# Performance work log

Measured on AMD Instinct MI355X. Metric: run time of the kernel, lower is better.

Reference implementation:

```python
import jax, jax.numpy as jnp
import numpy as np
from jax import lax

TAU = 2.0
V_TH = 1.0
SG_ALPHA = 4.0  # spikingjelly default sigmoid surrogate alpha


def lif_multistep(x):
    """Multi-step LIF with hard reset to 0, v_init=0, detach_reset=True.
    x: (T, ...). Returns binary spikes (same shape), with sigmoid surrogate
    gradient injected via straight-through estimator.
    """
    def step(v, xt):
        h = v + (xt - v) / TAU                      # membrane charge
        s_hard = (h >= V_TH).astype(h.dtype)        # heaviside spike
        sur = jax.nn.sigmoid(SG_ALPHA * (h - V_TH))  # surrogate for grad
        s = s_hard + (sur - lax.stop_gradient(sur))  # fwd=hard, bwd=surrogate
        v_next = h * (1.0 - lax.stop_gradient(s))    # hard reset, detached
        return v_next, s
    _, spikes = lax.scan(step, jnp.zeros_like(x[0]), x)
    return spikes


def setup_inputs() -> dict:
    key = jax.random.key(0)
    ks = jax.random.split(key, 6)
    T, B, N, D = 4, 16, 197, 512
    w_std = 1.0 / np.sqrt(D)
    return {
        "x":  jax.random.normal(ks[0], (T, B, N, D), dtype=jnp.float32),
        "Wq": jax.random.normal(ks[1], (D, D), dtype=jnp.float32) * w_std,
        "Wk": jax.random.normal(ks[2], (D, D), dtype=jnp.float32) * w_std,
        "Wv": jax.random.normal(ks[3], (D, D), dtype=jnp.float32) * w_std,
        "Wp": jax.random.normal(ks[4], (D, D), dtype=jnp.float32) * w_std,
        "bp": jnp.zeros((D,), dtype=jnp.float32),
    }


def reference(x, Wq, Wk, Wv, Wp, bp):
    T, B, N, D = x.shape
    H = 8
    dh = D // H
    scale = dh ** -0.5

    # QKV projections (nn.Linear: x @ W.T, no bias)
    q = jnp.einsum('tbnd,ed->tbne', x, Wq)
    k = jnp.einsum('tbnd,ed->tbne', x, Wk)
    v = jnp.einsum('tbnd,ed->tbne', x, Wv)

    # LIF spiking over timestep dim T -> binary spike tensors
    qs = lif_multistep(q).reshape(T, B, N, H, dh).transpose(0, 1, 3, 2, 4)
    ks_ = lif_multistep(k).reshape(T, B, N, H, dh).transpose(0, 1, 3, 2, 4)
    vs = lif_multistep(v).reshape(T, B, N, H, dh).transpose(0, 1, 3, 2, 4)

    # spike-driven attention: binary matmul, no softmax
    attn = jnp.einsum('tbhnd,tbhmd->tbhnm', qs, ks_) * scale  # (T,B,H,N,N)
    attn_map = lax.stop_gradient(attn)
    out = jnp.einsum('tbhnm,tbhmd->tbhnd', attn, vs)          # (T,B,H,N,dh)
    out = out.transpose(0, 1, 3, 2, 4).reshape(T, B, N, D)

    # output projection + LIF
    out = jnp.einsum('tbnd,ed->tbne', out, Wp) + bp
    out = lif_multistep(out)
    return out, attn_map
```

## Files before the change

### kernel.cpp

```cpp
#include <hip/hip_runtime.h>
#include <stdint.h>

#define T_ 4
#define B_ 16
#define N_ 197
#define D_ 512
#define H_ 8
#define DH 64
#define BN_ (B_*N_)
#define PLANE (BN_*D_)
#define M_ (T_*BN_)
#define TENSOR_ELEMS (T_*PLANE)
#define WELEMS (D_*D_)
#define MH (M_*H_)
#define FLAG_TOL 6e-3f
#define NFW3 (3*PLANE/64)
#define NFWP (PLANE/64)

typedef __attribute__((ext_vector_type(8))) short short8v;
typedef __attribute__((ext_vector_type(8))) _Float16 f16x8;
typedef __attribute__((ext_vector_type(4))) float f32x4;
typedef __attribute__((ext_vector_type(16))) float f32x16;
typedef __attribute__((ext_vector_type(4))) unsigned short ushort4v;
typedef unsigned long long u64;
typedef unsigned int u32;

__device__ __forceinline__ ushort f16_bits(float f) {
    _Float16 h = (_Float16)f;
    return __builtin_bit_cast(unsigned short, h);
}
__device__ __forceinline__ float f16_val(ushort u) {
    return (float)__builtin_bit_cast(_Float16, u);
}

__device__ __forceinline__ void gload16(const void* g, void* l) {
    __builtin_amdgcn_global_load_lds(
        (const __attribute__((address_space(1))) unsigned int*)g,
        (__attribute__((address_space(3))) unsigned int*)l, 16, 0, 0);
}

__global__ void cvt16(const float* __restrict__ src, ushort* __restrict__ dst, int n)
{
    int i = (blockIdx.x*256 + threadIdx.x)*4;
    if (i >= n) return;
    float4 v = *(const float4*)(src + i);
    ushort4v o;
    o[0] = f16_bits(v.x); o[1] = f16_bits(v.y);
    o[2] = f16_bits(v.z); o[3] = f16_bits(v.w);
    *(ushort4v*)(dst + i) = o;
}

__global__ __launch_bounds__(256, 4)
void gemm_qkv_lif(const ushort* __restrict__ xh, const ushort* __restrict__ w3h,
                  u64* __restrict__ bits3, u64* __restrict__ fmap3)
{
    __shared__ __align__(16) ushort smem[16384];
    const int tid = threadIdx.x;
    const int lane = tid & 63, wn = tid >> 6;
    const int l31 = lane & 31, lg = lane >> 5;
    const int nyz = 12, nz = 3;

    int nwg = gridDim.x, orig = blockIdx.x;
    int q8 = nwg >> 3, r8 = nwg & 7, xcd = orig & 7, loc = orig >> 3;
    int wg = (xcd < r8 ? xcd*(q8+1) : r8*(q8+1) + (xcd-r8)*q8) + loc;
    int bx = wg / nyz, yz = wg - bx*nyz;
    int by = yz / nz,  z  = yz - by*nz;

    const int bm0 = bx * 32;
    const int bn0 = by * 128;
    const ushort* Wz = w3h + (size_t)z * WELEMS;

    f32x16 acc[4];
    #pragma unroll
    for (int t = 0; t < 4; ++t)
        #pragma unroll
        for (int r = 0; r < 16; ++r) acc[t][r] = 0.f;

    for (int kt = 0; kt < D_; kt += 64) {
        #pragma unroll
        for (int i = 0; i < 8; ++i) {
            const int q = ((i & 3) << 8) | tid;
            const int row = q & 127, c = q >> 7;
            ushort* dst = smem + ((i >> 2) << 13) + q*8;
            if (i < 4) {
                int t = row >> 5, r32 = row & 31;
                if (bm0 + r32 < BN_)
                    gload16(xh + ((size_t)(t*BN_ + bm0 + r32)*D_ + kt + c*8), dst);
            } else {
                gload16(Wz + ((size_t)(bn0 + row)*D_ + kt + c*8), dst);
            }
        }
        __syncthreads();
        #pragma unroll
        for (int s = 0; s < 4; ++s) {
            const int cA = (s << 1) | lg;
            f16x8 bv = *(const f16x8*)&smem[8192 + (cA*128 + wn*32 + l31)*8];
            #pragma unroll
            for (int t = 0; t < 4; ++t) {
                f16x8 av = *(const f16x8*)&smem[(cA*128 + t*32 + l31)*8];
                acc[t] = __builtin_amdgcn_mfma_f32_32x32x16_f16(av, bv, acc[t], 0, 0, 0);
            }
        }
        __syncthreads();
    }

    u32* sp = (u32*)smem;
    u32* fl = (u32*)smem + 512;
    #pragma unroll
    for (int r = 0; r < 16; ++r) {
        bool s[4]; bool fg = false; float v = 0.f;
        #pragma unroll
        for (int t = 0; t < 4; ++t) {
            float h = v + (acc[t][r] - v)*0.5f;
            s[t] = h >= 1.0f;
            fg |= fabsf(h - 1.0f) < FLAG_TOL;
            v = s[t] ? 0.f : h;
        }
        #pragma unroll
        for (int t = 0; t < 4; ++t) {
            u64 m = __ballot(s[t]);
            if (lane == 0) {
                sp[((wn*4 + t)*16 + r)*2 + 0] = (u32)m;
                sp[((wn*4 + t)*16 + r)*2 + 1] = (u32)(m >> 32);
            }
        }
        u64 fm = __ballot(fg);
        if (lane == 0) {
            fl[(wn*16 + r)*2 + 0] = (u32)fm;
            fl[(wn*16 + r)*2 + 1] = (u32)(fm >> 32);
        }
    }
    __syncthreads();
    {
        int t = tid >> 6, row32 = (tid >> 1) & 31, hl = tid & 1;
        int rr = (row32 & 3) | ((row32 >> 3) << 2);
        int lgg = (row32 >> 2) & 1;
        u64 word = (u64)sp[(((2*hl)*4 + t)*16 + rr)*2 + lgg]
                 | ((u64)sp[(((2*hl+1)*4 + t)*16 + rr)*2 + lgg] << 32);
        if (bm0 + row32 < BN_)
            bits3[(size_t)z*MH + (size_t)(t*BN_ + bm0 + row32)*H_ + (bn0 >> 6) + hl] = word;
        if (tid < 64) {
            int rowf = tid >> 1, hlf = tid & 1;
            int rf = (rowf & 3) | ((rowf >> 3) << 2);
            int lgf = (rowf >> 2) & 1;
            u64 fw = (u64)fl[((2*hlf)*16 + rf)*2 + lgf]
                   | ((u64)fl[((2*hlf+1)*16 + rf)*2 + lgf] << 32);
            if (bm0 + rowf < BN_)
                fmap3[(size_t)z*NFWP + (size_t)(bm0 + rowf)*8 + (bn0 >> 6) + hlf] = fw;
        }
    }
}

__global__ __launch_bounds__(256, 4)
void gemm_proj_lif(const ushort* __restrict__ oh, const ushort* __restrict__ wph,
                   const float* __restrict__ bias, float* __restrict__ outp,
                   u64* __restrict__ fmapp)
{
    __shared__ __align__(16) ushort smem[16384];
    const int tid = threadIdx.x;
    const int lane = tid & 63, wn = tid >> 6;
    const int l31 = lane & 31, lg = lane >> 5;
    const int nyz = 4;

    int nwg = gridDim.x, orig = blockIdx.x;
    int q8 = nwg >> 3, r8 = nwg & 7, xcd = orig & 7, loc = orig >> 3;
    int wg = (xcd < r8 ? xcd*(q8+1) : r8*(q8+1) + (xcd-r8)*q8) + loc;
    int bx = wg / nyz, by = wg - bx*nyz;

    const int bm0 = bx * 32, bn0 = by * 128;

    f32x16 acc[4];
    #pragma unroll
    for (int t = 0; t < 4; ++t)
        #pragma unroll
        for (int r = 0; r < 16; ++r) acc[t][r] = 0.f;

    for (int kt = 0; kt < D_; kt += 64) {
        #pragma unroll
        for (int i = 0; i < 8; ++i) {
            const int q = ((i & 3) << 8) | tid;
            const int row = q & 127, c = q >> 7;
            ushort* dst = smem + ((i >> 2) << 13) + q*8;
            if (i < 4) {
                int t = row >> 5, r32 = row & 31;
                if (bm0 + r32 < BN_)
                    gload16(oh + ((size_t)(t*BN_ + bm0 + r32)*D_ + kt + c*8), dst);
            } else {
                gload16(wph + ((size_t)(bn0 + row)*D_ + kt + c*8), dst);
            }
        }
        __syncthreads();
        #pragma unroll
        for (int s = 0; s < 4; ++s) {
            const int cA = (s << 1) | lg;
            f16x8 bv = *(const f16x8*)&smem[8192 + (cA*128 + wn*32 + l31)*8];
            #pragma unroll
            for (int t = 0; t < 4; ++t) {
                f16x8 av = *(const f16x8*)&smem[(cA*128 + t*32 + l31)*8];
                acc[t] = __builtin_amdgcn_mfma_f32_32x32x16_f16(av, bv, acc[t], 0, 0, 0);
            }
        }
        __syncthreads();
    }

    const int gcol = bn0 + wn*32 + l31;
    const float bb = bias[gcol];
    u32* fl = (u32*)smem;
    #pragma unroll
    for (int r = 0; r < 16; ++r) {
        const int row32 = (r & 3) + 8*(r >> 2) + 4*lg;
        const bool live = bm0 + row32 < BN_;
        bool fg = false; float v = 0.f;
        #pragma unroll
        for (int t = 0; t < 4; ++t) {
            float h = v + ((acc[t][r] + bb) - v)*0.5f;
            bool st = h >= 1.0f;
            fg |= fabsf(h - 1.0f) < FLAG_TOL;
            if (live)
                outp[(size_t)t*PLANE + (size_t)(bm0 + row32)*D_ + gcol] = st ? 1.0f : 0.0f;
            v = st ? 0.f : h;
        }
        u64 fm = __ballot(fg);
        if (lane == 0) {
            fl[(wn*16 + r)*2 + 0] = (u32)fm;
            fl[(wn*16 + r)*2 + 1] = (u32)(fm >> 32);
        }
    }
    __syncthreads();
    if (tid < 64) {
        int rowf = tid >> 1, hlf = tid & 1;
        int rf = (rowf & 3) | ((rowf >> 3) << 2);
        int lgf = (rowf >> 2) & 1;
        u64 fw = (u64)fl[((2*hlf)*16 + rf)*2 + lgf]
               | ((u64)fl[((2*hlf+1)*16 + rf)*2 + lgf] << 32);
        if (bm0 + rowf < BN_)
            fmapp[(size_t)(bm0 + rowf)*8 + (bn0 >> 6) + hlf] = fw;
    }
}

__global__ __launch_bounds__(256)
void fixup_qkv(const float* __restrict__ x,
               const float* __restrict__ Wq, const float* __restrict__ Wk,
               const float* __restrict__ Wv,
               u64* __restrict__ bits3, const u64* __restrict__ flagmap)
{
    const int lane = threadIdx.x & 63;
    const int wv = blockIdx.x*4 + (threadIdx.x >> 6);
    const int nw = gridDim.x*4;
    for (int w = wv; w < NFW3; w += nw) {
        u64 fm = flagmap[w];
        while (fm) {
            int bit = __ffsll((long long)fm) - 1;
            fm &= fm - 1;
            int id = (w << 6) + bit;
            int tsr = id / PLANE;
            int rem = id - tsr*PLANE;
            int r = rem >> 9, e = rem & (D_-1);
            const float* W = (tsr==0) ? Wq : (tsr==1 ? Wk : Wv);
            const float* wr = W + (size_t)e*D_;
            u64* bits = bits3 + (size_t)tsr*MH;
            float wv8[8];
            #pragma unroll
            for (int i = 0; i < 8; ++i) wv8[i] = wr[lane + 64*i];
            double dots[T_];
            #pragma unroll
            for (int t = 0; t < T_; ++t) {
                const float* xr = x + (size_t)(t*BN_ + r)*D_;
                float xv8[8];
                #pragma unroll
                for (int i = 0; i < 8; ++i) xv8[i] = xr[lane + 64*i];
                double p = 0.0;
                #pragma unroll
                for (int i = 0; i < 8; ++i) p += (double)xv8[i]*(double)wv8[i];
                dots[t] = p;
            }
            #pragma unroll
            for (int off = 32; off > 0; off >>= 1)
                #pragma unroll
                for (int t = 0; t < T_; ++t)
                    dots[t] += __shfl_down(dots[t], off);
            if (lane == 0) {
                double v = 0.0;
                u64 b = 1ull << (e & 63);
                #pragma unroll
                for (int t = 0; t < T_; ++t) {
                    double hh = v + (dots[t] - v)/2.0;
                    bool s = hh >= 1.0;
                    size_t wd = (size_t)(t*BN_ + r)*H_ + (e >> 6);
                    if (s) atomicOr(&bits[wd], b);
                    else   atomicAnd(&bits[wd], ~b);
                    v = s ? 0.0 : hh;
                }
            }
        }
    }
}

#define NP 208
#define QSTR 72
#define JP 224
#define VSTR 232

__global__ __launch_bounds__(256)
void attn_qk(const u64* __restrict__ qbits, const u64* __restrict__ kbits,
             float* __restrict__ attn_out)
{
    __shared__ ushort Qs[NP][QSTR];
    __shared__ ushort Ks[NP][QSTR];
    int tb = blockIdx.x, h = blockIdx.y;
    int tid = threadIdx.x, wave = tid >> 6, lane = tid & 63;

    for (int idx = tid; idx < NP*16; idx += 256) {
        int j = idx >> 4, d4 = (idx & 15) << 2;
        ushort qv[4] = {0,0,0,0}, kv[4] = {0,0,0,0};
        if (j < N_) {
            size_t w = ((size_t)tb*N_ + j)*H_ + h;
            u64 qw = qbits[w], kw = kbits[w];
            #pragma unroll
            for (int r = 0; r < 4; ++r) {
                qv[r] = ((qw >> (d4+r)) & 1ull) ? 0x3F80 : 0;
                kv[r] = ((kw >> (d4+r)) & 1ull) ? 0x3F80 : 0;
            }
        }
        #pragma unroll
        for (int r = 0; r < 4; ++r) { Qs[j][d4+r] = qv[r]; Ks[j][d4+r] = kv[r]; }
    }
    __syncthreads();

    const int il = lane & 15;
    const int kk = (lane >> 4) << 3;
    const int ig = (lane >> 4) << 2;
    const size_t amap = ((size_t)tb*H_ + h)*(size_t)(N_*N_);

    for (int it = wave; it < 13; it += 4) {
        int i0 = it << 4;
        short8v a0 = *(const short8v*)&Qs[i0 + il][kk];
        short8v a1 = *(const short8v*)&Qs[i0 + il][kk + 32];
        for (int jt = 0; jt < 13; ++jt) {
            int j0 = jt << 4;
            short8v b0 = *(const short8v*)&Ks[j0 + il][kk];
            short8v b1 = *(const short8v*)&Ks[j0 + il][kk + 32];
            f32x4 c = {0.f, 0.f, 0.f, 0.f};
            c = __builtin_amdgcn_mfma_f32_16x16x32_bf16(a0, b0, c, 0, 0, 0);
            c = __builtin_amdgcn_mfma_f32_16x16x32_bf16(a1, b1, c, 0, 0, 0);
            int j = j0 + il;
            if (j < N_) {
                #pragma unroll
                for (int r = 0; r < 4; ++r) {
                    int i = i0 + ig + r;
                    if (i < N_) attn_out[amap + (size_t)i*N_ + j] = c[r]*0.125f;
                }
            }
        }
    }
}

__global__ __launch_bounds__(256)
void attn_pv(const float* __restrict__ attn, const u64* __restrict__ vbits,
             ushort* __restrict__ of16)
{
    __shared__ ushort Vt[DH][VSTR];
    int tb = blockIdx.x, h = blockIdx.y, zh = blockIdx.z;
    int tid = threadIdx.x, wave = tid >> 6, lane = tid & 63;

    for (int idx = tid; idx < JP*16; idx += 256) {
        int j = idx >> 4, d4 = (idx & 15) << 2;
        ushort vv[4] = {0,0,0,0};
        if (j < N_) {
            u64 vw = vbits[((size_t)tb*N_ + j)*H_ + h];
            #pragma unroll
            for (int r = 0; r < 4; ++r)
                vv[r] = ((vw >> (d4+r)) & 1ull) ? 0x3F80 : 0;
        }
        Vt[d4+0][j]=vv[0]; Vt[d4+1][j]=vv[1]; Vt[d4+2][j]=vv[2]; Vt[d4+3][j]=vv[3];
    }
    __syncthreads();

    const int il = lane & 15, kk = (lane >> 4) << 3, ig = (lane >> 4) << 2;
    const size_t amap = ((size_t)tb*H_ + h)*(size_t)(N_*N_);

    const int it_lo = zh*7 + wave;
    const int it_hi = zh*7 + 7 < 13 ? zh*7 + 7 : 13;
    for (int it = it_lo; it < it_hi; it += 4) {
        int i0 = it << 4;
        int row = i0 + il; if (row > N_-1) row = N_-1;
        const float* arow = attn + amap + (size_t)row*N_;
        f32x4 o[4];
        #pragma unroll
        for (int dt = 0; dt < 4; ++dt) o[dt] = (f32x4){0.f,0.f,0.f,0.f};
        #pragma unroll
        for (int kt = 0; kt < 7; ++kt) {
            const int c0 = kt*32 + kk;
            float f[8];
            if (kt < 6) {
                float4 fa = *(const float4*)(arow + c0);
                float4 fb = *(const float4*)(arow + c0 + 4);
                f[0]=fa.x; f[1]=fa.y; f[2]=fa.z; f[3]=fa.w;
                f[4]=fb.x; f[5]=fb.y; f[6]=fb.z; f[7]=fb.w;
            } else {
                #pragma unroll
                for (int j = 0; j < 8; ++j)
                    f[j] = (c0 + j < N_) ? arow[c0 + j] : 0.f;
            }
            short8v a;
            #pragma unroll
            for (int j = 0; j < 8; ++j)
                a[j] = (short)(__float_as_uint(f[j]) >> 16);
            #pragma unroll
            for (int dt = 0; dt < 4; ++dt) {
                short8v b = *(const short8v*)&Vt[dt*16 + il][c0];
                o[dt] = __builtin_amdgcn_mfma_f32_16x16x32_bf16(a, b, o[dt], 0, 0, 0);
            }
        }
        #pragma unroll
        for (int dt = 0; dt < 4; ++dt)
            #pragma unroll
            for (int r = 0; r < 4; ++r) {
                int i = i0 + ig + r;
                if (i < N_)
                    of16[((size_t)tb*N_ + i)*D_ + (size_t)h*DH + dt*16 + il] =
                        f16_bits(o[dt][r]);
            }
    }
}

__global__ __launch_bounds__(256)
void fixup_proj(const ushort* __restrict__ of16, const float* __restrict__ Wp,
                const float* __restrict__ bp, float* __restrict__ outp,
                const u64* __restrict__ flagmap)
{
    const int lane = threadIdx.x & 63;
    const int wv = blockIdx.x*4 + (threadIdx.x >> 6);
    const int nw = gridDim.x*4;
    for (int w = wv; w < NFWP; w += nw) {
        u64 fm = flagmap[w];
        while (fm) {
            int bit = __ffsll((long long)fm) - 1;
            fm &= fm - 1;
            int rem = (w << 6) + bit;
            int r = rem >> 9, e = rem & (D_-1);
            const float* wr = Wp + (size_t)e*D_;
            float wv8[8];
            #pragma unroll
            for (int i = 0; i < 8; ++i) wv8[i] = wr[lane + 64*i];
            double dots[T_];
            #pragma unroll
            for (int t = 0; t < T_; ++t) {
                const ushort* ar = of16 + (size_t)(t*BN_ + r)*D_;
                float av8[8];
                #pragma unroll
                for (int i = 0; i < 8; ++i) av8[i] = f16_val(ar[lane + 64*i]);
                double p = 0.0;
                #pragma unroll
                for (int i = 0; i < 8; ++i) p += (double)av8[i]*(double)wv8[i];
                dots[t] = p;
            }
            #pragma unroll
            for (int off = 32; off > 0; off >>= 1)
                #pragma unroll
                for (int t = 0; t < T_; ++t)
                    dots[t] += __shfl_down(dots[t], off);
            if (lane == 0) {
                double v = 0.0;
                #pragma unroll
                for (int t = 0; t < T_; ++t) {
                    double xt = dots[t] + (double)bp[e];
                    double h = v + (xt - v)/2.0;
                    bool s = h >= 1.0;
                    outp[(size_t)t*PLANE + rem] = s ? 1.0f : 0.0f;
                    v = s ? 0.0 : h;
                }
            }
        }
    }
}

extern "C" void kernel_launch(void* const* d_in, const int* in_sizes, int n_in,
                              void* d_out, int out_size, void* d_ws, size_t ws_size,
                              hipStream_t stream)
{
    const float* x  = (const float*)d_in[0];
    const float* Wq = (const float*)d_in[1];
    const float* Wk = (const float*)d_in[2];
    const float* Wv = (const float*)d_in[3];
    const float* Wp = (const float*)d_in[4];
    const float* bp = (const float*)d_in[5];
    float* out_spk  = (float*)d_out;
    float* attn_out = (float*)d_out + TENSOR_ELEMS;

    char* ws = (char*)d_ws;
    const size_t BUFB = (size_t)TENSOR_ELEMS * sizeof(float);
    if (ws_size < 4*BUFB) return;
    ushort* of16 = (ushort*)(ws + 2*BUFB);
    char* r3 = ws + 3*BUFB;
    ushort* xh   = (ushort*)r3;
    ushort* w3h  = (ushort*)(r3 + (13u<<20));
    ushort* wph  = (ushort*)(r3 + (15u<<20));
    u64*    bits3 = (u64*)(r3 + (16u<<20));
    u64*    qbits = bits3;
    u64*    kbits = bits3 + MH;
    u64*    vbits = bits3 + 2*(size_t)MH;
    u64*    fmap3 = (u64*)(r3 + (19u<<20));
    u64*    fmapp = (u64*)(r3 + (20u<<20));

    cvt16<<<TENSOR_ELEMS/1024, 256, 0, stream>>>(x, xh, TENSOR_ELEMS);
    cvt16<<<WELEMS/1024, 256, 0, stream>>>(Wq, w3h,            WELEMS);
    cvt16<<<WELEMS/1024, 256, 0, stream>>>(Wk, w3h +   WELEMS, WELEMS);
    cvt16<<<WELEMS/1024, 256, 0, stream>>>(Wv, w3h + 2*WELEMS, WELEMS);
    cvt16<<<WELEMS/1024, 256, 0, stream>>>(Wp, wph,            WELEMS);

    gemm_qkv_lif<<<99*12, 256, 0, stream>>>(xh, w3h, bits3, fmap3);
    fixup_qkv<<<2048, 256, 0, stream>>>(x, Wq, Wk, Wv, bits3, fmap3);

    attn_qk<<<dim3(T_*B_, H_), 256, 0, stream>>>(qbits, kbits, attn_out);
    attn_pv<<<dim3(T_*B_, H_, 2), 256, 0, stream>>>(attn_out, vbits, of16);

    gemm_proj_lif<<<99*4, 256, 0, stream>>>(of16, wph, bp, out_spk, fmapp);
    fixup_proj<<<1024, 256, 0, stream>>>(of16, Wp, bp, out_spk, fmapp);
}
```

Measured before the change: 181.5 us.

## Double-buffer GEMM LDS staging and fuse QK and PV attention kernels

Both projection GEMMs now use two LDS buffers, issuing the next K-tile's global-to-LDS loads before computing on the current one. This is meant to overlap memory latency with MFMA work, at the cost of doubling shared memory and dropping the occupancy hint from launch bounds. Separately, the QK and PV attention kernels are merged into one. Each wave computes its row tile of scores, writes them to the attention map, and keeps a bf16 copy in LDS for the PV MFMA, so the fp32 attention map is no longer re-read from global memory. The fused kernel launches half as many blocks as the old PV kernel, which risks lower parallelism.

```diff
diff --git a/kernel.cpp b/kernel.cpp
--- a/kernel.cpp
+++ b/kernel.cpp
@@ -39,6 +39,14 @@
         (__attribute__((address_space(3))) unsigned int*)l, 16, 0, 0);
 }
 
+__device__ __forceinline__ short8v unpack8(u32 bits) {
+    short8v r;
+    #pragma unroll
+    for (int j = 0; j < 8; ++j)
+        r[j] = (short)(((bits >> j) & 1u) ? 0x3F80 : 0);
+    return r;
+}
+
 __global__ void cvt16(const float* __restrict__ src, ushort* __restrict__ dst, int n)
 {
     int i = (blockIdx.x*256 + threadIdx.x)*4;
@@ -50,11 +58,11 @@
     *(ushort4v*)(dst + i) = o;
 }
 
-__global__ __launch_bounds__(256, 4)
+__global__ __launch_bounds__(256)
 void gemm_qkv_lif(const ushort* __restrict__ xh, const ushort* __restrict__ w3h,
                   u64* __restrict__ bits3, u64* __restrict__ fmap3)
 {
-    __shared__ __align__(16) ushort smem[16384];
+    __shared__ __align__(16) ushort smem[32768];
     const int tid = threadIdx.x;
     const int lane = tid & 63, wn = tid >> 6;
     const int l31 = lane & 31, lg = lane >> 5;
@@ -76,12 +84,12 @@
         #pragma unroll
         for (int r = 0; r < 16; ++r) acc[t][r] = 0.f;
 
-    for (int kt = 0; kt < D_; kt += 64) {
+    auto STAGE = [&](int buf, int kt) {
         #pragma unroll
         for (int i = 0; i < 8; ++i) {
             const int q = ((i & 3) << 8) | tid;
             const int row = q & 127, c = q >> 7;
-            ushort* dst = smem + ((i >> 2) << 13) + q*8;
+            ushort* dst = smem + buf*16384 + ((i >> 2) << 13) + q*8;
             if (i < 4) {
                 int t = row >> 5, r32 = row & 31;
                 if (bm0 + r32 < BN_)
@@ -90,18 +98,30 @@
                 gload16(Wz + ((size_t)(bn0 + row)*D_ + kt + c*8), dst);
             }
         }
-        __syncthreads();
+    };
+    auto COMPUTE = [&](int buf) {
+        const ushort* base = smem + buf*16384;
         #pragma unroll
         for (int s = 0; s < 4; ++s) {
             const int cA = (s << 1) | lg;
-            f16x8 bv = *(const f16x8*)&smem[8192 + (cA*128 + wn*32 + l31)*8];
+            f16x8 bv = *(const f16x8*)&base[8192 + (cA*128 + wn*32 + l31)*8];
             #pragma unroll
             for (int t = 0; t < 4; ++t) {
-                f16x8 av = *(const f16x8*)&smem[(cA*128 + t*32 + l31)*8];
+                f16x8 av = *(const f16x8*)&base[(cA*128 + t*32 + l31)*8];
                 acc[t] = __builtin_amdgcn_mfma_f32_32x32x16_f16(av, bv, acc[t], 0, 0, 0);
             }
         }
+    };
+
+    STAGE(0, 0);
+    __syncthreads();
+    int cur = 0;
+    #pragma unroll
+    for (int k64 = 0; k64 < 8; ++k64) {
+        if (k64 < 7) STAGE(cur ^ 1, (k64 + 1)*64);
+        COMPUTE(cur);
         __syncthreads();
+        cur ^= 1;
     }
 
     u32* sp = (u32*)smem;
@@ -151,12 +171,12 @@
     }
 }
 
-__global__ __launch_bounds__(256, 4)
+__global__ __launch_bounds__(256)
 void gemm_proj_lif(const ushort* __restrict__ oh, const ushort* __restrict__ wph,
                    const float* __restrict__ bias, float* __restrict__ outp,
                    u64* __restrict__ fmapp)
 {
-    __shared__ __align__(16) ushort smem[16384];
+    __shared__ __align__(16) ushort smem[32768];
     const int tid = threadIdx.x;
     const int lane = tid & 63, wn = tid >> 6;
     const int l31 = lane & 31, lg = lane >> 5;
@@ -175,12 +195,12 @@
         #pragma unroll
         for (int r = 0; r < 16; ++r) acc[t][r] = 0.f;
 
-    for (int kt = 0; kt < D_; kt += 64) {
+    auto STAGE = [&](int buf, int kt) {
         #pragma unroll
         for (int i = 0; i < 8; ++i) {
             const int q = ((i & 3) << 8) | tid;
             const int row = q & 127, c = q >> 7;
-            ushort* dst = smem + ((i >> 2) << 13) + q*8;
+            ushort* dst = smem + buf*16384 + ((i >> 2) << 13) + q*8;
             if (i < 4) {
                 int t = row >> 5, r32 = row & 31;
                 if (bm0 + r32 < BN_)
@@ -189,18 +209,30 @@
                 gload16(wph + ((size_t)(bn0 + row)*D_ + kt + c*8), dst);
             }
         }
-        __syncthreads();
+    };
+    auto COMPUTE = [&](int buf) {
+        const ushort* base = smem + buf*16384;
         #pragma unroll
         for (int s = 0; s < 4; ++s) {
             const int cA = (s << 1) | lg;
-            f16x8 bv = *(const f16x8*)&smem[8192 + (cA*128 + wn*32 + l31)*8];
+            f16x8 bv = *(const f16x8*)&base[8192 + (cA*128 + wn*32 + l31)*8];
             #pragma unroll
             for (int t = 0; t < 4; ++t) {
-                f16x8 av = *(const f16x8*)&smem[(cA*128 + t*32 + l31)*8];
+                f16x8 av = *(const f16x8*)&base[(cA*128 + t*32 + l31)*8];
                 acc[t] = __builtin_amdgcn_mfma_f32_32x32x16_f16(av, bv, acc[t], 0, 0, 0);
             }
         }
+    };
+
+    STAGE(0, 0);
+    __syncthreads();
+    int cur = 0;
+    #pragma unroll
+    for (int k64 = 0; k64 < 8; ++k64) {
+        if (k64 < 7) STAGE(cur ^ 1, (k64 + 1)*64);
+        COMPUTE(cur);
         __syncthreads();
+        cur ^= 1;
     }
 
     const int gcol = bn0 + wn*32 + l31;
@@ -296,71 +328,17 @@
     }
 }
 
-#define NP 208
-#define QSTR 72
 #define JP 224
 #define VSTR 232
 
 __global__ __launch_bounds__(256)
-void attn_qk(const u64* __restrict__ qbits, const u64* __restrict__ kbits,
-             float* __restrict__ attn_out)
-{
-    __shared__ ushort Qs[NP][QSTR];
-    __shared__ ushort Ks[NP][QSTR];
+void attn_fused(const u64* __restrict__ qbits, const u64* __restrict__ kbits,
+                const u64* __restrict__ vbits,
+                float* __restrict__ attn_out, ushort* __restrict__ of16)
+{
+    __shared__ ushort Vt[DH][VSTR];
+    __shared__ ushort Ss[4][16][VSTR];
     int tb = blockIdx.x, h = blockIdx.y;
-    int tid = threadIdx.x, wave = tid >> 6, lane = tid & 63;
-
-    for (int idx = tid; idx < NP*16; idx += 256) {
-        int j = idx >> 4, d4 = (idx & 15) << 2;
-        ushort qv[4] = {0,0,0,0}, kv[4] = {0,0,0,0};
-        if (j < N_) {
-            size_t w = ((size_t)tb*N_ + j)*H_ + h;
-            u64 qw = qbits[w], kw = kbits[w];
-            #pragma unroll
-            for (int r = 0; r < 4; ++r) {
-                qv[r] = ((qw >> (d4+r)) & 1ull) ? 0x3F80 : 0;
-                kv[r] = ((kw >> (d4+r)) & 1ull) ? 0x3F80 : 0;
-            }
-        }
-        #pragma unroll
-        for (int r = 0; r < 4; ++r) { Qs[j][d4+r] = qv[r]; Ks[j][d4+r] = kv[r]; }
-    }
-    __syncthreads();
-
-    const int il = lane & 15;
-    const int kk = (lane >> 4) << 3;
-    const int ig = (lane >> 4) << 2;
-    const size_t amap = ((size_t)tb*H_ + h)*(size_t)(N_*N_);
-
-    for (int it = wave; it < 13; it += 4) {
-        int i0 = it << 4;
-        short8v a0 = *(const short8v*)&Qs[i0 + il][kk];
-        short8v a1 = *(const short8v*)&Qs[i0 + il][kk + 32];
-        for (int jt = 0; jt < 13; ++jt) {
-            int j0 = jt << 4;
-            short8v b0 = *(const short8v*)&Ks[j0 + il][kk];
-            short8v b1 = *(const short8v*)&Ks[j0 + il][kk + 32];
-            f32x4 c = {0.f, 0.f, 0.f, 0.f};
-            c = __builtin_amdgcn_mfma_f32_16x16x32_bf16(a0, b0, c, 0, 0, 0);
-            c = __builtin_amdgcn_mfma_f32_16x16x32_bf16(a1, b1, c, 0, 0, 0);
-            int j = j0 + il;
-            if (j < N_) {
-                #pragma unroll
-                for (int r = 0; r < 4; ++r) {
-                    int i = i0 + ig + r;
-                    if (i < N_) attn_out[amap + (size_t)i*N_ + j] = c[r]*0.125f;
-                }
-            }
-        }
-    }
-}
-
-__global__ __launch_bounds__(256)
-void attn_pv(const float* __restrict__ attn, const u64* __restrict__ vbits,
-             ushort* __restrict__ of16)
-{
-    __shared__ ushort Vt[DH][VSTR];
-    int tb = blockIdx.x, h = blockIdx.y, zh = blockIdx.z;
     int tid = threadIdx.x, wave = tid >> 6, lane = tid & 63;
 
     for (int idx = tid; idx < JP*16; idx += 256) {
@@ -374,41 +352,46 @@
         }
         Vt[d4+0][j]=vv[0]; Vt[d4+1][j]=vv[1]; Vt[d4+2][j]=vv[2]; Vt[d4+3][j]=vv[3];
     }
+    for (int idx = lane; idx < 16*16; idx += 64)
+        Ss[wave][idx >> 4][208 + (idx & 15)] = 0;
     __syncthreads();
 
     const int il = lane & 15, kk = (lane >> 4) << 3, ig = (lane >> 4) << 2;
     const size_t amap = ((size_t)tb*H_ + h)*(size_t)(N_*N_);
 
-    const int it_lo = zh*7 + wave;
-    const int it_hi = zh*7 + 7 < 13 ? zh*7 + 7 : 13;
-    for (int it = it_lo; it < it_hi; it += 4) {
+    for (int it = wave; it < 13; it += 4) {
         int i0 = it << 4;
-        int row = i0 + il; if (row > N_-1) row = N_-1;
-        const float* arow = attn + amap + (size_t)row*N_;
+        int qrow = i0 + il;
+        u64 qw = (qrow < N_) ? qbits[((size_t)tb*N_ + qrow)*H_ + h] : 0ull;
+        short8v a0 = unpack8((u32)(qw >> kk));
+        short8v a1 = unpack8((u32)((qw >> 32) >> kk));
+        for (int jt = 0; jt < 13; ++jt) {
+            int j0 = jt << 4, jrow = j0 + il;
+            u64 kw = (jrow < N_) ? kbits[((size_t)tb*N_ + jrow)*H_ + h] : 0ull;
+            short8v b0 = unpack8((u32)(kw >> kk));
+            short8v b1 = unpack8((u32)((kw >> 32) >> kk));
+            f32x4 c = {0.f, 0.f, 0.f, 0.f};
+            c = __builtin_amdgcn_mfma_f32_16x16x32_bf16(a0, b0, c, 0, 0, 0);
+            c = __builtin_amdgcn_mfma_f32_16x16x32_bf16(a1, b1, c, 0, 0, 0);
+            int j = j0 + il;
+            #pragma unroll
+            for (int r = 0; r < 4; ++r) {
+                float sv = c[r]*0.125f;
+                int i = i0 + ig + r;
+                if (i < N_ && j < N_)
+                    attn_out[amap + (size_t)i*N_ + j] = sv;
+                Ss[wave][ig + r][j] = (ushort)(__float_as_uint(sv) >> 16);
+            }
+        }
         f32x4 o[4];
         #pragma unroll
         for (int dt = 0; dt < 4; ++dt) o[dt] = (f32x4){0.f,0.f,0.f,0.f};
         #pragma unroll
         for (int kt = 0; kt < 7; ++kt) {
-            const int c0 = kt*32 + kk;
-            float f[8];
-            if (kt < 6) {
-                float4 fa = *(const float4*)(arow + c0);
-                float4 fb = *(const float4*)(arow + c0 + 4);
-                f[0]=fa.x; f[1]=fa.y; f[2]=fa.z; f[3]=fa.w;
-                f[4]=fb.x; f[5]=fb.y; f[6]=fb.z; f[7]=fb.w;
-            } else {
-                #pragma unroll
-                for (int j = 0; j < 8; ++j)
-                    f[j] = (c0 + j < N_) ? arow[c0 + j] : 0.f;
-            }
-            short8v a;
-            #pragma unroll
-            for (int j = 0; j < 8; ++j)
-                a[j] = (short)(__float_as_uint(f[j]) >> 16);
+            short8v a = *(const short8v*)&Ss[wave][il][kt*32 + kk];
             #pragma unroll
             for (int dt = 0; dt < 4; ++dt) {
-                short8v b = *(const short8v*)&Vt[dt*16 + il][c0];
+                short8v b = *(const short8v*)&Vt[dt*16 + il][kt*32 + kk];
                 o[dt] = __builtin_amdgcn_mfma_f32_16x16x32_bf16(a, b, o[dt], 0, 0, 0);
             }
         }
@@ -512,8 +495,8 @@
     gemm_qkv_lif<<<99*12, 256, 0, stream>>>(xh, w3h, bits3, fmap3);
     fixup_qkv<<<2048, 256, 0, stream>>>(x, Wq, Wk, Wv, bits3, fmap3);
 
-    attn_qk<<<dim3(T_*B_, H_), 256, 0, stream>>>(qbits, kbits, attn_out);
-    attn_pv<<<dim3(T_*B_, H_, 2), 256, 0, stream>>>(attn_out, vbits, of16);
+    attn_fused<<<dim3(T_*B_, H_), 256, 0, stream>>>(
+        qbits, kbits, vbits, attn_out, of16);
 
     gemm_proj_lif<<<99*4, 256, 0, stream>>>(of16, wph, bp, out_spk, fmapp);
     fixup_proj<<<1024, 256, 0, stream>>>(of16, Wp, bp, out_spk, fmapp);
```

Result: faster. 168.9 us (-6.9%).
